# Optimization experiments

Hardware: AMD Instinct MI355X
Metric: run time of the kernel (lower is better)

Reference implementation:

```python
import jax, jax.numpy as jnp
import numpy as np

ALPHA = 8.3  # depth similarity sharpness, F_D = exp(-alpha*|D(p0)-D(pn)|) (depth-aware CNN)
PAD, STRIDE, DIL, KH, KW = 1, 1, 1, 3, 3


def setup_inputs() -> dict:
    key = jax.random.key(0)
    k1, k2, k3, k4 = jax.random.split(key, 4)
    B, C_in, C_out, H, W = 2, 32, 32, 512, 512
    x = jax.random.normal(k1, (B, C_in, H, W), dtype=jnp.float32)
    depth = jax.random.uniform(k2, (B, 1, H, W), dtype=jnp.float32)
    weight = jax.random.normal(k3, (C_out, C_in, KH, KW), dtype=jnp.float32) * 0.05
    bias = jax.random.normal(k4, (C_out,), dtype=jnp.float32) * 0.05
    return {"x": x, "depth": depth, "weight": weight, "bias": bias}


def _depthconv(x, depth, weight, bias):
    B, C, H, W = x.shape
    C_out = weight.shape[0]
    H_out = (H + 2 * PAD - DIL * (KH - 1) - 1) // STRIDE + 1
    W_out = (W + 2 * PAD - DIL * (KW - 1) - 1) // STRIDE + 1
    x_p = jnp.pad(x, ((0, 0), (0, 0), (PAD, PAD), (PAD, PAD)))
    d_p = jnp.pad(depth, ((0, 0), (0, 0), (PAD, PAD), (PAD, PAD)))
    # depth at the receptive-field center of each output pixel, [B,1,H_out,W_out]
    ci, cj = (KH // 2) * DIL, (KW // 2) * DIL
    d_c = d_p[:, :, ci:ci + H_out * STRIDE:STRIDE, cj:cj + W_out * STRIDE:STRIDE]
    out = jnp.broadcast_to(bias[None, :, None, None], (B, C_out, H_out, W_out)).astype(x.dtype)
    for ki in range(KH):
        for kj in range(KW):
            hs, ws = ki * DIL, kj * DIL
            xs = x_p[:, :, hs:hs + H_out * STRIDE:STRIDE, ws:ws + W_out * STRIDE:STRIDE]
            ds = d_p[:, :, hs:hs + H_out * STRIDE:STRIDE, ws:ws + W_out * STRIDE:STRIDE]
            sim = jnp.exp(-ALPHA * jnp.abs(d_c - ds))  # [B,1,H_out,W_out]
            out = out + jnp.einsum('oc,bchw->bohw', weight[:, :, ki, kj], xs * sim)
    return out


def reference(x, depth, weight, bias):
    return _depthconv(x, depth, weight, bias)
```

## Files before the change

### kernel.cpp

```cpp
#include <hip/hip_runtime.h>

typedef _Float16 half8 __attribute__((ext_vector_type(8)));
typedef float floatx4 __attribute__((ext_vector_type(4)));

constexpr int C  = 32, H = 512, W = 512, HW = H * W;
constexpr int Hp = 514, Wp = 514;
constexpr int NPX = 2 * Hp * Wp;

constexpr size_t XOFF = 0;
constexpr size_t XSZ  = (size_t)NPX * 64;
constexpr size_t DOFF = XOFF + XSZ;
constexpr size_t DSZ  = (size_t)NPX * 8;
constexpr size_t WOFF = DOFF + DSZ;

__device__ __forceinline__ unsigned pack2h(float lo, float hi) {
    unsigned a = (unsigned)__builtin_bit_cast(unsigned short, (_Float16)lo);
    unsigned b = (unsigned)__builtin_bit_cast(unsigned short, (_Float16)hi);
    return a | (b << 16);
}

__global__ __launch_bounds__(256) void pack_all(
    const float* __restrict__ x, const float* __restrict__ depth,
    const float* __restrict__ weight,
    unsigned* __restrict__ xp, float2* __restrict__ dpk, uint4* __restrict__ wp)
{
    const int bid = blockIdx.x;
    const int tid = threadIdx.x;

    if (bid >= 2048) {
        if (bid < 2065) {
            int i = (bid - 2048) * 256 + tid;
            if (i >= 4104) return;
            int b = i / 2052, r = i % 2052;
            int hh, ww;
            if (r < 514)       { hh = 0;   ww = r; }
            else if (r < 1028) { hh = 513; ww = r - 514; }
            else { int j = r - 1028; hh = 1 + (j >> 1); ww = (j & 1) ? 513 : 0; }
            size_t ppx = ((size_t)(b * Hp + hh)) * Wp + ww;
            uint4 z = {0u, 0u, 0u, 0u};
            uint4* p = (uint4*)(xp + ppx * 16);
            p[0] = z; p[1] = z; p[2] = z; p[3] = z;
            dpk[ppx] = make_float2(0.f, 0.f);
        } else {
            int j = (bid - 2065) * 256 + tid;
            if (j >= 1152) return;
            int lane = j & 63, half = (j >> 6) & 1, tap = j >> 7;
            int o = half * 16 + (lane & 15), q = lane >> 4;
            uint4 v;
            v.x = pack2h(weight[(o * 32 + q * 8 + 0) * 9 + tap], weight[(o * 32 + q * 8 + 1) * 9 + tap]);
            v.y = pack2h(weight[(o * 32 + q * 8 + 2) * 9 + tap], weight[(o * 32 + q * 8 + 3) * 9 + tap]);
            v.z = pack2h(weight[(o * 32 + q * 8 + 4) * 9 + tap], weight[(o * 32 + q * 8 + 5) * 9 + tap]);
            v.w = pack2h(weight[(o * 32 + q * 8 + 6) * 9 + tap], weight[(o * 32 + q * 8 + 7) * 9 + tap]);
            wp[j] = v;
        }
        return;
    }

    __shared__ float t[4][32][65];
    const int wseg = bid & 7, hseg = (bid >> 3) & 127, b = bid >> 10;
    const int h0 = hseg * 4, w0 = wseg * 64;

    const float* xb = x + (size_t)b * C * HW + h0 * W + w0;
    #pragma unroll
    for (int p = 0; p < 8; ++p) {
        int slot = p * 256 + tid;
        int r = slot >> 9, c = (slot >> 4) & 31, f4 = slot & 15;
        float4 v = *(const float4*)(xb + (size_t)c * HW + r * W + f4 * 4);
        t[r][c][f4 * 4 + 0] = v.x; t[r][c][f4 * 4 + 1] = v.y;
        t[r][c][f4 * 4 + 2] = v.z; t[r][c][f4 * 4 + 3] = v.w;
    }

    {
        int rr = tid >> 6, ww = tid & 63;
        float d = depth[(size_t)b * HW + (h0 + rr) * W + w0 + ww];
        size_t ppx = ((size_t)(b * Hp + h0 + rr + 1)) * Wp + (w0 + 1 + ww);
        dpk[ppx] = make_float2(__expf(-8.3f * d), __expf(8.3f * d));
    }
    __syncthreads();

    const int px = tid >> 2, q = tid & 3;
    #pragma unroll
    for (int r = 0; r < 4; ++r) {
        uint4 o;
        o.x = pack2h(t[r][q * 8 + 0][px], t[r][q * 8 + 1][px]);
        o.y = pack2h(t[r][q * 8 + 2][px], t[r][q * 8 + 3][px]);
        o.z = pack2h(t[r][q * 8 + 4][px], t[r][q * 8 + 5][px]);
        o.w = pack2h(t[r][q * 8 + 6][px], t[r][q * 8 + 7][px]);
        size_t ppx = ((size_t)(b * Hp + h0 + r + 1)) * Wp + (w0 + 1 + px);
        *(uint4*)(xp + ppx * 16 + q * 4) = o;
    }
}

__global__ __launch_bounds__(256) void depthconv_main(
    const unsigned* __restrict__ xp,
    const float2*   __restrict__ dpk,
    const uint4*    __restrict__ wp,
    const float*    __restrict__ bias,
    float*          __restrict__ out)
{
    const int bid  = blockIdx.x;
    const int wseg = bid & 7, h = (bid >> 3) & 511, b = bid >> 12;
    const int lane = threadIdx.x & 63, wid = threadIdx.x >> 6;
    const int nn   = lane & 15, q = lane >> 4;
    const int pw   = wseg * 64 + wid * 16 + nn;

    half8 af[2][9];
    #pragma unroll
    for (int tap = 0; tap < 9; ++tap) {
        af[0][tap] = __builtin_bit_cast(half8, wp[(tap * 2 + 0) * 64 + lane]);
        af[1][tap] = __builtin_bit_cast(half8, wp[(tap * 2 + 1) * 64 + lane]);
    }

    floatx4 acc0, acc1;
    #pragma unroll
    for (int r = 0; r < 4; ++r) {
        acc0[r] = bias[q * 4 + r];
        acc1[r] = bias[16 + q * 4 + r];
    }

    const size_t rowbase = ((size_t)(b * Hp + h)) * Wp + pw;
    const float2 dc = dpk[rowbase + Wp + 1];

    #pragma unroll
    for (int ki = 0; ki < 3; ++ki) {
        #pragma unroll
        for (int kj = 0; kj < 3; ++kj) {
            const int tap = ki * 3 + kj;
            const size_t np = rowbase + (size_t)ki * Wp + kj;
            float2 dn = dpk[np];
            float s = fminf(dn.y * dc.x, dn.x * dc.y);
            _Float16 hs = (_Float16)s;
            half8 sv = { hs, hs, hs, hs, hs, hs, hs, hs };

            half8 xv = __builtin_bit_cast(half8, *(const uint4*)(xp + np * 16 + q * 4));
            half8 bfrag = xv * sv;

            acc0 = __builtin_amdgcn_mfma_f32_16x16x32_f16(af[0][tap], bfrag, acc0, 0, 0, 0);
            acc1 = __builtin_amdgcn_mfma_f32_16x16x32_f16(af[1][tap], bfrag, acc1, 0, 0, 0);
        }
    }

    float* op = out + (size_t)b * C * HW + h * W + pw;
    #pragma unroll
    for (int r = 0; r < 4; ++r) {
        op[(size_t)(q * 4 + r) * HW]        = acc0[r];
        op[(size_t)(16 + q * 4 + r) * HW]   = acc1[r];
    }
}

extern "C" void kernel_launch(void* const* d_in, const int* in_sizes, int n_in,
                              void* d_out, int out_size, void* d_ws, size_t ws_size,
                              hipStream_t stream) {
    const float* x      = (const float*)d_in[0];
    const float* depth  = (const float*)d_in[1];
    const float* weight = (const float*)d_in[2];
    const float* bias   = (const float*)d_in[3];
    float* out          = (float*)d_out;

    unsigned* xp  = (unsigned*)((char*)d_ws + XOFF);
    float2*   dpk = (float2*)  ((char*)d_ws + DOFF);
    uint4*    wpk = (uint4*)   ((char*)d_ws + WOFF);

    hipLaunchKernelGGL(pack_all, dim3(2070), dim3(256), 0, stream,
                       x, depth, weight, xp, dpk, wpk);
    hipLaunchKernelGGL(depthconv_main, dim3(2 * 512 * 8), dim3(256), 0, stream,
                       xp, dpk, wpk, bias, out);
}
```

Before: 160.0 us.

## Fuse input packing into conv kernel with LDS halo tile and row reuse

Removes the separate packing pass that wrote a padded fp16 copy of x and a depth-similarity buffer to global memory. Each block now loads an 8x64 output tile plus its halo from x and depth straight into LDS, converting to fp16 and applying a swizzle there. It then walks 10 input rows and reuses each loaded row across the up to three output rows that need it. The cost is 16 accumulator vectors per thread, which raises register pressure (launch bounds set to 2 blocks per unit), and a 25% halo overhead on global loads.

```diff
diff --git a/kernel.cpp b/kernel.cpp
--- a/kernel.cpp
+++ b/kernel.cpp
@@ -3,15 +3,10 @@
 typedef _Float16 half8 __attribute__((ext_vector_type(8)));
 typedef float floatx4 __attribute__((ext_vector_type(4)));
 
-constexpr int C  = 32, H = 512, W = 512, HW = H * W;
-constexpr int Hp = 514, Wp = 514;
-constexpr int NPX = 2 * Hp * Wp;
-
-constexpr size_t XOFF = 0;
-constexpr size_t XSZ  = (size_t)NPX * 64;
-constexpr size_t DOFF = XOFF + XSZ;
-constexpr size_t DSZ  = (size_t)NPX * 8;
-constexpr size_t WOFF = DOFF + DSZ;
+constexpr int C = 32, H = 512, W = 512, HW = H * W;
+constexpr int TBH = 8, TBW = 64;
+constexpr int RR  = TBH + 2;
+constexpr int PX  = 72;
 
 __device__ __forceinline__ unsigned pack2h(float lo, float hi) {
     unsigned a = (unsigned)__builtin_bit_cast(unsigned short, (_Float16)lo);
@@ -19,90 +14,69 @@
     return a | (b << 16);
 }
 
-__global__ __launch_bounds__(256) void pack_all(
+__global__ __launch_bounds__(256) void pack_w(const float* __restrict__ weight,
+                                              uint4* __restrict__ wp) {
+    int j = blockIdx.x * 256 + threadIdx.x;
+    if (j >= 1152) return;
+    int lane = j & 63, half = (j >> 6) & 1, tap = j >> 7;
+    int o = half * 16 + (lane & 15), q = lane >> 4;
+    uint4 v;
+    v.x = pack2h(weight[(o * 32 + q * 8 + 0) * 9 + tap], weight[(o * 32 + q * 8 + 1) * 9 + tap]);
+    v.y = pack2h(weight[(o * 32 + q * 8 + 2) * 9 + tap], weight[(o * 32 + q * 8 + 3) * 9 + tap]);
+    v.z = pack2h(weight[(o * 32 + q * 8 + 4) * 9 + tap], weight[(o * 32 + q * 8 + 5) * 9 + tap]);
+    v.w = pack2h(weight[(o * 32 + q * 8 + 6) * 9 + tap], weight[(o * 32 + q * 8 + 7) * 9 + tap]);
+    wp[j] = v;
+}
+
+__global__ __launch_bounds__(256, 2) void depthconv_fused(
     const float* __restrict__ x, const float* __restrict__ depth,
-    const float* __restrict__ weight,
-    unsigned* __restrict__ xp, float2* __restrict__ dpk, uint4* __restrict__ wp)
+    const uint4* __restrict__ wp, const float* __restrict__ bias,
+    float* __restrict__ out)
 {
-    const int bid = blockIdx.x;
+    __shared__ __attribute__((aligned(16))) unsigned xsl[RR * PX * 16];
+    __shared__ float2 dsim[RR][PX];
+
+    const int bid  = blockIdx.x;
+    const int wseg = bid & 7, hseg = (bid >> 3) & 63, b = bid >> 9;
+    const int h0 = hseg * TBH, w0 = wseg * TBW;
     const int tid = threadIdx.x;
 
-    if (bid >= 2048) {
-        if (bid < 2065) {
-            int i = (bid - 2048) * 256 + tid;
-            if (i >= 4104) return;
-            int b = i / 2052, r = i % 2052;
-            int hh, ww;
-            if (r < 514)       { hh = 0;   ww = r; }
-            else if (r < 1028) { hh = 513; ww = r - 514; }
-            else { int j = r - 1028; hh = 1 + (j >> 1); ww = (j & 1) ? 513 : 0; }
-            size_t ppx = ((size_t)(b * Hp + hh)) * Wp + ww;
-            uint4 z = {0u, 0u, 0u, 0u};
-            uint4* p = (uint4*)(xp + ppx * 16);
-            p[0] = z; p[1] = z; p[2] = z; p[3] = z;
-            dpk[ppx] = make_float2(0.f, 0.f);
-        } else {
-            int j = (bid - 2065) * 256 + tid;
-            if (j >= 1152) return;
-            int lane = j & 63, half = (j >> 6) & 1, tap = j >> 7;
-            int o = half * 16 + (lane & 15), q = lane >> 4;
-            uint4 v;
-            v.x = pack2h(weight[(o * 32 + q * 8 + 0) * 9 + tap], weight[(o * 32 + q * 8 + 1) * 9 + tap]);
-            v.y = pack2h(weight[(o * 32 + q * 8 + 2) * 9 + tap], weight[(o * 32 + q * 8 + 3) * 9 + tap]);
-            v.z = pack2h(weight[(o * 32 + q * 8 + 4) * 9 + tap], weight[(o * 32 + q * 8 + 5) * 9 + tap]);
-            v.w = pack2h(weight[(o * 32 + q * 8 + 6) * 9 + tap], weight[(o * 32 + q * 8 + 7) * 9 + tap]);
-            wp[j] = v;
+    for (int u = tid; u < 16 * RR * 18; u += 256) {
+        int f4 = u % 18, t = u / 18;
+        int r = t % RR, cp = t / RR;
+        int h = h0 - 1 + r, wst = w0 - 4 + f4 * 4;
+        bool valid = (h >= 0) && (h < H) && (wst >= 0) && (wst < W);
+        float4 va = {0.f, 0.f, 0.f, 0.f}, vb = {0.f, 0.f, 0.f, 0.f};
+        if (valid) {
+            const float* xb = x + ((size_t)(b * C + 2 * cp)) * HW + h * W + wst;
+            va = *(const float4*)xb;
+            vb = *(const float4*)(xb + HW);
         }
-        return;
+        int swz = (((cp >> 2) ^ (f4 & 3)) << 2) | (cp & 3);
+        unsigned* dst = &xsl[(r * PX + f4 * 4) * 16 + swz];
+        dst[0]  = pack2h(va.x, vb.x);
+        dst[16] = pack2h(va.y, vb.y);
+        dst[32] = pack2h(va.z, vb.z);
+        dst[48] = pack2h(va.w, vb.w);
     }
 
-    __shared__ float t[4][32][65];
-    const int wseg = bid & 7, hseg = (bid >> 3) & 127, b = bid >> 10;
-    const int h0 = hseg * 4, w0 = wseg * 64;
-
-    const float* xb = x + (size_t)b * C * HW + h0 * W + w0;
-    #pragma unroll
-    for (int p = 0; p < 8; ++p) {
-        int slot = p * 256 + tid;
-        int r = slot >> 9, c = (slot >> 4) & 31, f4 = slot & 15;
-        float4 v = *(const float4*)(xb + (size_t)c * HW + r * W + f4 * 4);
-        t[r][c][f4 * 4 + 0] = v.x; t[r][c][f4 * 4 + 1] = v.y;
-        t[r][c][f4 * 4 + 2] = v.z; t[r][c][f4 * 4 + 3] = v.w;
+    if (tid < RR * 18) {
+        int f4 = tid % 18, r = tid / 18;
+        int h = h0 - 1 + r, wst = w0 - 4 + f4 * 4;
+        bool valid = (h >= 0) && (h < H) && (wst >= 0) && (wst < W);
+        float4 dv = {0.f, 0.f, 0.f, 0.f};
+        if (valid) dv = *(const float4*)(depth + (size_t)b * HW + h * W + wst);
+        float dd[4] = {dv.x, dv.y, dv.z, dv.w};
+        #pragma unroll
+        for (int j = 0; j < 4; ++j) {
+            dsim[r][f4 * 4 + j] = valid
+                ? make_float2(__expf(-8.3f * dd[j]), __expf(8.3f * dd[j]))
+                : make_float2(0.f, 0.f);
+        }
     }
 
-    {
-        int rr = tid >> 6, ww = tid & 63;
-        float d = depth[(size_t)b * HW + (h0 + rr) * W + w0 + ww];
-        size_t ppx = ((size_t)(b * Hp + h0 + rr + 1)) * Wp + (w0 + 1 + ww);
-        dpk[ppx] = make_float2(__expf(-8.3f * d), __expf(8.3f * d));
-    }
-    __syncthreads();
-
-    const int px = tid >> 2, q = tid & 3;
-    #pragma unroll
-    for (int r = 0; r < 4; ++r) {
-        uint4 o;
-        o.x = pack2h(t[r][q * 8 + 0][px], t[r][q * 8 + 1][px]);
-        o.y = pack2h(t[r][q * 8 + 2][px], t[r][q * 8 + 3][px]);
-        o.z = pack2h(t[r][q * 8 + 4][px], t[r][q * 8 + 5][px]);
-        o.w = pack2h(t[r][q * 8 + 6][px], t[r][q * 8 + 7][px]);
-        size_t ppx = ((size_t)(b * Hp + h0 + r + 1)) * Wp + (w0 + 1 + px);
-        *(uint4*)(xp + ppx * 16 + q * 4) = o;
-    }
-}
-
-__global__ __launch_bounds__(256) void depthconv_main(
-    const unsigned* __restrict__ xp,
-    const float2*   __restrict__ dpk,
-    const uint4*    __restrict__ wp,
-    const float*    __restrict__ bias,
-    float*          __restrict__ out)
-{
-    const int bid  = blockIdx.x;
-    const int wseg = bid & 7, h = (bid >> 3) & 511, b = bid >> 12;
-    const int lane = threadIdx.x & 63, wid = threadIdx.x >> 6;
-    const int nn   = lane & 15, q = lane >> 4;
-    const int pw   = wseg * 64 + wid * 16 + nn;
+    const int lane = tid & 63, wid = tid >> 6;
+    const int nn = lane & 15, q = lane >> 4;
 
     half8 af[2][9];
     #pragma unroll
@@ -111,40 +85,57 @@
         af[1][tap] = __builtin_bit_cast(half8, wp[(tap * 2 + 1) * 64 + lane]);
     }
 
-    floatx4 acc0, acc1;
+    floatx4 acc[TBH][2];
     #pragma unroll
-    for (int r = 0; r < 4; ++r) {
-        acc0[r] = bias[q * 4 + r];
-        acc1[r] = bias[16 + q * 4 + r];
-    }
+    for (int o = 0; o < TBH; ++o)
+        #pragma unroll
+        for (int i = 0; i < 4; ++i) {
+            acc[o][0][i] = bias[q * 4 + i];
+            acc[o][1][i] = bias[16 + q * 4 + i];
+        }
 
-    const size_t rowbase = ((size_t)(b * Hp + h)) * Wp + pw;
-    const float2 dc = dpk[rowbase + Wp + 1];
+    __syncthreads();
+
+    const int pc = wid * 16 + nn;
+    float2 dc[TBH];
+    #pragma unroll
+    for (int o = 0; o < TBH; ++o) dc[o] = dsim[o + 1][pc + 4];
 
     #pragma unroll
-    for (int ki = 0; ki < 3; ++ki) {
+    for (int r = 0; r < RR; ++r) {
+        uint4 xraw[3]; float2 dn[3];
         #pragma unroll
         for (int kj = 0; kj < 3; ++kj) {
-            const int tap = ki * 3 + kj;
-            const size_t np = rowbase + (size_t)ki * Wp + kj;
-            float2 dn = dpk[np];
-            float s = fminf(dn.y * dc.x, dn.x * dc.y);
-            _Float16 hs = (_Float16)s;
-            half8 sv = { hs, hs, hs, hs, hs, hs, hs, hs };
-
-            half8 xv = __builtin_bit_cast(half8, *(const uint4*)(xp + np * 16 + q * 4));
-            half8 bfrag = xv * sv;
-
-            acc0 = __builtin_amdgcn_mfma_f32_16x16x32_f16(af[0][tap], bfrag, acc0, 0, 0, 0);
-            acc1 = __builtin_amdgcn_mfma_f32_16x16x32_f16(af[1][tap], bfrag, acc1, 0, 0, 0);
+            int p = pc + 3 + kj;
+            xraw[kj] = *(const uint4*)&xsl[(r * PX + p) * 16 + ((q ^ ((p >> 2) & 3)) << 2)];
+            dn[kj] = dsim[r][p];
+        }
+        #pragma unroll
+        for (int kj = 0; kj < 3; ++kj) {
+            #pragma unroll
+            for (int ki = 0; ki < 3; ++ki) {
+                int o = r - ki;
+                if (o < 0 || o >= TBH) continue;
+                int tap = ki * 3 + kj;
+                float s = fminf(dn[kj].y * dc[o].x, dn[kj].x * dc[o].y);
+                _Float16 hs = (_Float16)s;
+                half8 sv = { hs, hs, hs, hs, hs, hs, hs, hs };
+                half8 bf = __builtin_bit_cast(half8, xraw[kj]) * sv;
+                acc[o][0] = __builtin_amdgcn_mfma_f32_16x16x32_f16(af[0][tap], bf, acc[o][0], 0, 0, 0);
+                acc[o][1] = __builtin_amdgcn_mfma_f32_16x16x32_f16(af[1][tap], bf, acc[o][1], 0, 0, 0);
+            }
         }
     }
 
-    float* op = out + (size_t)b * C * HW + h * W + pw;
+    const int pw = w0 + pc;
     #pragma unroll
-    for (int r = 0; r < 4; ++r) {
-        op[(size_t)(q * 4 + r) * HW]        = acc0[r];
-        op[(size_t)(16 + q * 4 + r) * HW]   = acc1[r];
+    for (int o = 0; o < TBH; ++o) {
+        float* op = out + (size_t)b * C * HW + (size_t)(h0 + o) * W + pw;
+        #pragma unroll
+        for (int i = 0; i < 4; ++i) {
+            op[(size_t)(q * 4 + i) * HW]      = acc[o][0][i];
+            op[(size_t)(16 + q * 4 + i) * HW] = acc[o][1][i];
+        }
     }
 }
 
@@ -157,12 +148,9 @@
     const float* bias   = (const float*)d_in[3];
     float* out          = (float*)d_out;
 
-    unsigned* xp  = (unsigned*)((char*)d_ws + XOFF);
-    float2*   dpk = (float2*)  ((char*)d_ws + DOFF);
-    uint4*    wpk = (uint4*)   ((char*)d_ws + WOFF);
+    uint4* wpk = (uint4*)d_ws;
 
-    hipLaunchKernelGGL(pack_all, dim3(2070), dim3(256), 0, stream,
-                       x, depth, weight, xp, dpk, wpk);
-    hipLaunchKernelGGL(depthconv_main, dim3(2 * 512 * 8), dim3(256), 0, stream,
-                       xp, dpk, wpk, bias, out);
+    hipLaunchKernelGGL(pack_w, dim3(5), dim3(256), 0, stream, weight, wpk);
+    hipLaunchKernelGGL(depthconv_fused, dim3(2 * 64 * 8), dim3(256), 0, stream,
+                       x, depth, wpk, bias, out);
 }
```

Measured after the change: 142.5 us. -11.0%, faster.
